# Performance work log

Hardware: AMD Instinct MI355X
Metric: run time of the kernel (lower is better)

## Reference

```python
import jax, jax.numpy as jnp
import numpy as np

BATCH, FEAT, NUM, K = 8, 512, 512, 32

def _l2norm(v, axis):
    # matches F.normalize(p=2): v / max(||v||, eps)
    n = jnp.sqrt(jnp.sum(v * v, axis=axis, keepdims=True))
    return v / jnp.maximum(n, 1e-12)

def setup_inputs() -> dict:
    key = jax.random.key(0)
    k1, k2, k3, k4 = jax.random.split(key, 4)
    x = jax.random.normal(k1, (BATCH, FEAT, NUM), dtype=jnp.float32)
    W = jax.random.normal(k2, (K, FEAT), dtype=jnp.float32) * 0.02
    b = jnp.zeros((K,), dtype=jnp.float32)
    mu = jax.random.uniform(k3, (FEAT, K), dtype=jnp.float32)
    # sigma drawn away from 0 to keep the 1/sigma division well-conditioned
    sigma = jax.random.uniform(k4, (FEAT, K), dtype=jnp.float32, minval=0.5, maxval=1.0)
    return {"x": x, "W": W, "b": b, "mu": mu, "sigma": sigma}

def reference(x, W, b, mu, sigma):
    batch, feat, num = x.shape
    xt = jnp.transpose(x, (0, 2, 1))                      # [b, n, f]
    a = jax.nn.softmax(xt @ W.T + b, axis=2)              # [b, n, k]
    # Fused reduction over n: f = (x - mu)/sigma, fv1 = sum_n a*f, fv2 = sum_n a*(f^2-1)
    asum = jnp.sum(a, axis=1)                             # [b, k]
    ax = jnp.einsum('bnk,bnf->bfk', a, xt)                # sum_n a * x
    ax2 = jnp.einsum('bnk,bnf->bfk', a, xt * xt)          # sum_n a * x^2
    mu_b = mu[None]                                       # [1, f, k]
    sig_b = sigma[None]
    asum_b = asum[:, None, :]                             # [b, 1, k]
    fv1 = (ax - mu_b * asum_b) / sig_b                    # [b, f, k]
    fv2 = (ax2 - 2.0 * mu_b * ax + mu_b * mu_b * asum_b) / (sig_b * sig_b) - asum_b
    fv1 = _l2norm(fv1, 2).reshape(batch, -1)
    fv1 = _l2norm(fv1, 1)
    fv2 = _l2norm(fv2, 2).reshape(batch, -1)
    fv2 = _l2norm(fv2, 1)
    return jnp.concatenate([fv1, fv2], axis=1)            # [b, 2*f*k]
```

## Files before the change

### kernel.cpp

```cpp
#include <hip/hip_runtime.h>


#define B_ 8
#define F_ 512
#define N_ 512
#define K_ 32

__global__ __launch_bounds__(256) void k_a(const float* __restrict__ x,
                                           const float* __restrict__ W,
                                           const float* __restrict__ bias,
                                           float* __restrict__ aP,
                                           float* __restrict__ asumP) {
  __shared__ float xs[128][18];
  __shared__ float ws[128 * 32];
  __shared__ float red2[16][516];
  __shared__ float sm4[4][32];
  const int t = threadIdx.x;
  const int b  = blockIdx.x >> 5;
  const int nt = blockIdx.x & 31;
  const int n0 = nt << 4;
  const int ng = t & 3;
  const int kg = (t >> 2) & 3;
  const int fs = t >> 4;
  const int n4 = ng * 4;
  const int k8 = kg * 8;

  float acc[4][8];
#pragma unroll
  for (int i = 0; i < 4; ++i)
#pragma unroll
    for (int j = 0; j < 8; ++j) acc[i][j] = 0.f;

  float xr[8], wr[16];
#pragma unroll
  for (int it = 0; it < 8; ++it) {
    int flat = t + 256 * it;
    xr[it] = x[(size_t)(b * F_ + (flat >> 4)) * N_ + n0 + (flat & 15)];
  }
#pragma unroll
  for (int it = 0; it < 16; ++it) {
    int flat = t + 256 * it;
    wr[it] = W[(flat >> 7) * F_ + (flat & 127)];
  }
#pragma unroll
  for (int it = 0; it < 8; ++it) {
    int flat = t + 256 * it;
    xs[flat >> 4][flat & 15] = xr[it];
  }
#pragma unroll
  for (int it = 0; it < 16; ++it) {
    int flat = t + 256 * it;
    int f = flat & 127, k = flat >> 7;
    ws[f * 32 + (k ^ (f & 31))] = wr[it];
  }
  __syncthreads();

  for (int ph = 0; ph < 4; ++ph) {
    if (ph < 3) {
      const int fb = (ph + 1) << 7;
#pragma unroll
      for (int it = 0; it < 8; ++it) {
        int flat = t + 256 * it;
        xr[it] = x[(size_t)(b * F_ + fb + (flat >> 4)) * N_ + n0 + (flat & 15)];
      }
#pragma unroll
      for (int it = 0; it < 16; ++it) {
        int flat = t + 256 * it;
        wr[it] = W[(flat >> 7) * F_ + fb + (flat & 127)];
      }
    }
#pragma unroll
    for (int fi = 0; fi < 8; ++fi) {
      const int f = fs * 8 + fi;
      const float2 x01 = *(const float2*)&xs[f][n4];
      const float2 x23 = *(const float2*)&xs[f][n4 + 2];
      const float4 wA = *(const float4*)&ws[f * 32 + ((k8) ^ (f & 28))];
      const float4 wB = *(const float4*)&ws[f * 32 + ((k8 + 4) ^ (f & 28))];
      const float xv[4] = {x01.x, x01.y, x23.x, x23.y};
      const float wa[4] = {((const float*)&wA)[0 ^ (fi & 3)],
                           ((const float*)&wA)[1 ^ (fi & 3)],
                           ((const float*)&wA)[2 ^ (fi & 3)],
                           ((const float*)&wA)[3 ^ (fi & 3)]};
      const float wb[4] = {((const float*)&wB)[0 ^ (fi & 3)],
                           ((const float*)&wB)[1 ^ (fi & 3)],
                           ((const float*)&wB)[2 ^ (fi & 3)],
                           ((const float*)&wB)[3 ^ (fi & 3)]};
#pragma unroll
      for (int i = 0; i < 4; ++i)
#pragma unroll
        for (int j = 0; j < 4; ++j) {
          acc[i][j]     += xv[i] * wa[j];
          acc[i][4 + j] += xv[i] * wb[j];
        }
    }
    __syncthreads();
    if (ph < 3) {
#pragma unroll
      for (int it = 0; it < 8; ++it) {
        int flat = t + 256 * it;
        xs[flat >> 4][flat & 15] = xr[it];
      }
#pragma unroll
      for (int it = 0; it < 16; ++it) {
        int flat = t + 256 * it;
        int f = flat & 127, k = flat >> 7;
        ws[f * 32 + (k ^ (f & 31))] = wr[it];
      }
      __syncthreads();
    }
  }

#pragma unroll
  for (int i = 0; i < 4; ++i) {
    float4 v1, v2;
    v1.x = acc[i][0]; v1.y = acc[i][1]; v1.z = acc[i][2]; v1.w = acc[i][3];
    v2.x = acc[i][4]; v2.y = acc[i][5]; v2.z = acc[i][6]; v2.w = acc[i][7];
    *(float4*)&red2[fs][(n4 + i) * 32 + k8] = v1;
    *(float4*)&red2[fs][(n4 + i) * 32 + k8 + 4] = v2;
  }
  __syncthreads();

  const int o0 = 2 * t;
  const int row = t >> 4;
  const int k0 = o0 & 31;
  float l0 = bias[k0], l1 = bias[k0 + 1];
#pragma unroll
  for (int s2 = 0; s2 < 16; ++s2) {
    float2 r = *(const float2*)&red2[s2][o0];
    l0 += r.x; l1 += r.y;
  }
  float m = fmaxf(l0, l1);
  m = fmaxf(m, __shfl_xor(m, 1));
  m = fmaxf(m, __shfl_xor(m, 2));
  m = fmaxf(m, __shfl_xor(m, 4));
  m = fmaxf(m, __shfl_xor(m, 8));
  const float e0 = __expf(l0 - m), e1 = __expf(l1 - m);
  float ssum = e0 + e1;
  ssum += __shfl_xor(ssum, 1);
  ssum += __shfl_xor(ssum, 2);
  ssum += __shfl_xor(ssum, 4);
  ssum += __shfl_xor(ssum, 8);
  const float inv = 1.f / ssum;
  const float a0 = e0 * inv, a1 = e1 * inv;
  float2 av; av.x = a0; av.y = a1;
  *(float2*)&aP[(size_t)(b * N_ + n0 + row) * K_ + k0] = av;

  float s0 = a0 + __shfl_xor(a0, 16); s0 += __shfl_xor(s0, 32);
  float s1 = a1 + __shfl_xor(a1, 16); s1 += __shfl_xor(s1, 32);
  const int l = t & 63, w = t >> 6;
  if (l < 16) { sm4[w][2 * l] = s0; sm4[w][2 * l + 1] = s1; }
  __syncthreads();
  if (t < 32) {
    float tot = sm4[0][t] + sm4[1][t] + sm4[2][t] + sm4[3][t];
    asumP[(b * 32 + nt) * 32 + t] = tot;
  }
}

__global__ __launch_bounds__(256) void k_ax(const float* __restrict__ x,
                                            const float* __restrict__ aP,
                                            float* __restrict__ axP,
                                            float* __restrict__ ax2P) {
  __shared__ float xsT[64 * 128];
  __shared__ float as_[64][36];
  const int t  = threadIdx.x;
  const int s  = blockIdx.x & 7;
  const int ft = (blockIdx.x >> 3) & 3;
  const int b  = blockIdx.x >> 5;
  const int f0 = ft << 7;
  const int n0 = s << 6;
  const int fg = t >> 3, kg = t & 7;
  const int f4 = fg * 4, k4 = kg * 4;

#pragma unroll
  for (int it = 0; it < 32; ++it) {
    int flat = t + 256 * it;
    int f = flat >> 6, nn = flat & 63;
    xsT[nn * 128 + (f ^ (nn & 31))] =
        x[(size_t)(b * F_ + f0 + f) * N_ + n0 + nn];
  }
#pragma unroll
  for (int it = 0; it < 8; ++it) {
    int flat = t + 256 * it;
    int r = flat >> 5, kk = flat & 31;
    as_[r][kk] = aP[(size_t)(b * N_ + n0 + r) * K_ + kk];
  }
  __syncthreads();

  float ax[4][4] = {{0.f}}, bx[4][4] = {{0.f}};
#pragma unroll 2
  for (int nb = 0; nb < 64; nb += 4) {
#pragma unroll
    for (int u = 0; u < 4; ++u) {
      const int n = nb + u;
      const float4 xv = *(const float4*)&xsT[n * 128 + (f4 ^ (n & 28))];
      const float4 av = *(const float4*)&as_[n][k4];
      const float* xp = (const float*)&xv;
      const float* ap = (const float*)&av;
#pragma unroll
      for (int i = 0; i < 4; ++i) {
        const float xi = xp[i ^ u];
        const float xq = xi * xi;
#pragma unroll
        for (int j = 0; j < 4; ++j) {
          ax[i][j] += xi * ap[j];
          bx[i][j] += xq * ap[j];
        }
      }
    }
  }

  const size_t pbase = ((size_t)(s * B_ + b) * F_ + f0 + f4) * K_ + k4;
#pragma unroll
  for (int i = 0; i < 4; ++i) {
    float4 v1, v2;
    v1.x = ax[i][0]; v1.y = ax[i][1]; v1.z = ax[i][2]; v1.w = ax[i][3];
    v2.x = bx[i][0]; v2.y = bx[i][1]; v2.z = bx[i][2]; v2.w = bx[i][3];
    *(float4*)&axP [pbase + (size_t)i * K_] = v1;
    *(float4*)&ax2P[pbase + (size_t)i * K_] = v2;
  }
}

__global__ __launch_bounds__(256) void k_fv(const float* __restrict__ axP,
                                            const float* __restrict__ ax2P,
                                            const float* __restrict__ asumP,
                                            const float* __restrict__ mu,
                                            const float* __restrict__ sg,
                                            float* __restrict__ out) {
  __shared__ float sm[32];
  const int t = threadIdx.x;
  const int g = blockIdx.x * 256 + t;
  const int k = g & 31;
  const int f = (g >> 5) & (F_ - 1);
  const int b = g >> 14;

  if (t < 32) {
    float s = 0.f;
#pragma unroll
    for (int nt = 0; nt < 32; ++nt) s += asumP[(b * 32 + nt) * 32 + t];
    sm[t] = s;
  }
  __syncthreads();

  float ax = 0.f, ax2 = 0.f;
#pragma unroll
  for (int s = 0; s < 8; ++s) {
    ax  += axP [(size_t)((s * B_ + b) * F_ + f) * K_ + k];
    ax2 += ax2P[(size_t)((s * B_ + b) * F_ + f) * K_ + k];
  }
  const float m  = mu[f * K_ + k];
  const float sd = sg[f * K_ + k];
  const float as = sm[k];

  const float fv1 = (ax - m * as) / sd;
  const float fv2 = (ax2 - 2.f * m * ax + m * m * as) / (sd * sd) - as;

  float s1 = fv1 * fv1, s2 = fv2 * fv2;
#pragma unroll
  for (int off = 16; off >= 1; off >>= 1) {
    s1 += __shfl_xor(s1, off, 32);
    s2 += __shfl_xor(s2, off, 32);
  }
  const float inv512 = 0.04419417382415922f;
  const float o1 = fv1 / fmaxf(sqrtf(s1), 1e-12f) * inv512;
  const float o2 = fv2 / fmaxf(sqrtf(s2), 1e-12f) * inv512;

  out[(size_t)b * (2 * F_ * K_) + f * K_ + k] = o1;
  out[(size_t)b * (2 * F_ * K_) + F_ * K_ + f * K_ + k] = o2;
}

extern "C" void kernel_launch(void* const* d_in, const int* in_sizes, int n_in,
                              void* d_out, int out_size, void* d_ws, size_t ws_size,
                              hipStream_t stream) {
  const float* x  = (const float*)d_in[0];
  const float* W  = (const float*)d_in[1];
  const float* bv = (const float*)d_in[2];
  const float* mu = (const float*)d_in[3];
  const float* sg = (const float*)d_in[4];
  float* out = (float*)d_out;

  float* ws    = (float*)d_ws;
  float* aP    = ws;
  float* axP   = ws + 131072;
  float* ax2P  = ws + 131072 + 1048576;
  float* asumP = ws + 131072 + 2 * 1048576;

  hipLaunchKernelGGL(k_a,  dim3(256), dim3(256), 0, stream, x, W, bv, aP, asumP);
  hipLaunchKernelGGL(k_ax, dim3(256), dim3(256), 0, stream, x, aP, axP, ax2P);
  hipLaunchKernelGGL(k_fv, dim3(512), dim3(256), 0, stream,
                     axP, ax2P, asumP, mu, sg, out);
}
```

Baseline: 85.78 us.

## Fuse weighted-moment reduction with Fisher-vector normalization into one kernel

Merges the k_ax and k_fv kernels into a single k_axfv kernel. Each block now owns 8 features of one batch and loops over all 512 points in chunks of 128, register-prefetching the next chunk of x and the soft-assignment matrix while the current one is computed. Per-thread partials are reduced in shared memory, then normalized and written directly. This removes the 8-way split-N partial buffers, the global round-trip between the two kernels and one launch. In exchange, each block rereads the full per-batch assignment matrix (64 blocks per batch) and gets less parallelism per block along N.

```diff
diff --git a/kernel.cpp b/kernel.cpp
--- a/kernel.cpp
+++ b/kernel.cpp
@@ -156,49 +156,75 @@
   }
 }
 
-__global__ __launch_bounds__(256) void k_ax(const float* __restrict__ x,
-                                            const float* __restrict__ aP,
-                                            float* __restrict__ axP,
-                                            float* __restrict__ ax2P) {
-  __shared__ float xsT[64 * 128];
-  __shared__ float as_[64][36];
+__global__ __launch_bounds__(256) void k_axfv(const float* __restrict__ x,
+                                              const float* __restrict__ aP,
+                                              const float* __restrict__ asumP,
+                                              const float* __restrict__ mu,
+                                              const float* __restrict__ sg,
+                                              float* __restrict__ out) {
+  __shared__ float pool[8448];
+  __shared__ float sm[32];
+  float* xs  = pool;
+  float* as_ = pool + 1056;
   const int t  = threadIdx.x;
-  const int s  = blockIdx.x & 7;
-  const int ft = (blockIdx.x >> 3) & 3;
-  const int b  = blockIdx.x >> 5;
-  const int f0 = ft << 7;
-  const int n0 = s << 6;
-  const int fg = t >> 3, kg = t & 7;
-  const int f4 = fg * 4, k4 = kg * 4;
-
-#pragma unroll
-  for (int it = 0; it < 32; ++it) {
-    int flat = t + 256 * it;
-    int f = flat >> 6, nn = flat & 63;
-    xsT[nn * 128 + (f ^ (nn & 31))] =
-        x[(size_t)(b * F_ + f0 + f) * N_ + n0 + nn];
-  }
-#pragma unroll
-  for (int it = 0; it < 8; ++it) {
-    int flat = t + 256 * it;
-    int r = flat >> 5, kk = flat & 31;
-    as_[r][kk] = aP[(size_t)(b * N_ + n0 + r) * K_ + kk];
-  }
-  __syncthreads();
+  const int b  = blockIdx.x >> 6;
+  const int ft = blockIdx.x & 63;
+  const int f0 = ft << 3;
+  const int kg = t & 7;
+  const int fg = (t >> 3) & 1;
+  const int ns = t >> 4;
+  const int k4 = kg * 4;
+  const int f4 = fg * 4;
+
+  if (t < 32) {
+    float s = 0.f;
+#pragma unroll
+    for (int nt = 0; nt < 32; ++nt) s += asumP[(b * 32 + nt) * 32 + t];
+    sm[t] = s;
+  }
 
   float ax[4][4] = {{0.f}}, bx[4][4] = {{0.f}};
-#pragma unroll 2
-  for (int nb = 0; nb < 64; nb += 4) {
-#pragma unroll
-    for (int u = 0; u < 4; ++u) {
-      const int n = nb + u;
-      const float4 xv = *(const float4*)&xsT[n * 128 + (f4 ^ (n & 28))];
-      const float4 av = *(const float4*)&as_[n][k4];
-      const float* xp = (const float*)&xv;
+  float xr[4], ar[16];
+#pragma unroll
+  for (int it = 0; it < 4; ++it) {
+    int flat = t + 256 * it;
+    xr[it] = x[(size_t)(b * F_ + f0 + (flat >> 7)) * N_ + (flat & 127)];
+  }
+#pragma unroll
+  for (int it = 0; it < 16; ++it)
+    ar[it] = aP[(size_t)b * N_ * K_ + t + 256 * it];
+#pragma unroll
+  for (int it = 0; it < 4; ++it) {
+    int flat = t + 256 * it;
+    xs[(flat >> 7) * 132 + (flat & 127)] = xr[it];
+  }
+#pragma unroll
+  for (int it = 0; it < 16; ++it) as_[t + 256 * it] = ar[it];
+  __syncthreads();
+
+  for (int c = 0; c < 4; ++c) {
+    if (c < 3) {
+      const int nc = (c + 1) << 7;
+#pragma unroll
+      for (int it = 0; it < 4; ++it) {
+        int flat = t + 256 * it;
+        xr[it] = x[(size_t)(b * F_ + f0 + (flat >> 7)) * N_ + nc + (flat & 127)];
+      }
+#pragma unroll
+      for (int it = 0; it < 16; ++it)
+        ar[it] = aP[(size_t)b * N_ * K_ + nc * K_ + t + 256 * it];
+    }
+#pragma unroll
+    for (int u = 0; u < 8; ++u) {
+      const int n = ns * 8 + u;
+      const float4 av = *(const float4*)&as_[n * 32 + k4];
       const float* ap = (const float*)&av;
+      float xv[4];
+#pragma unroll
+      for (int i = 0; i < 4; ++i) xv[i] = xs[(f4 + i) * 132 + n];
 #pragma unroll
       for (int i = 0; i < 4; ++i) {
-        const float xi = xp[i ^ u];
+        const float xi = xv[i];
         const float xq = xi * xi;
 #pragma unroll
         for (int j = 0; j < 4; ++j) {
@@ -207,52 +233,43 @@
         }
       }
     }
-  }
-
-  const size_t pbase = ((size_t)(s * B_ + b) * F_ + f0 + f4) * K_ + k4;
+    __syncthreads();
+    if (c < 3) {
+#pragma unroll
+      for (int it = 0; it < 4; ++it) {
+        int flat = t + 256 * it;
+        xs[(flat >> 7) * 132 + (flat & 127)] = xr[it];
+      }
+#pragma unroll
+      for (int it = 0; it < 16; ++it) as_[t + 256 * it] = ar[it];
+      __syncthreads();
+    }
+  }
+
 #pragma unroll
   for (int i = 0; i < 4; ++i) {
     float4 v1, v2;
     v1.x = ax[i][0]; v1.y = ax[i][1]; v1.z = ax[i][2]; v1.w = ax[i][3];
     v2.x = bx[i][0]; v2.y = bx[i][1]; v2.z = bx[i][2]; v2.w = bx[i][3];
-    *(float4*)&axP [pbase + (size_t)i * K_] = v1;
-    *(float4*)&ax2P[pbase + (size_t)i * K_] = v2;
-  }
-}
-
-__global__ __launch_bounds__(256) void k_fv(const float* __restrict__ axP,
-                                            const float* __restrict__ ax2P,
-                                            const float* __restrict__ asumP,
-                                            const float* __restrict__ mu,
-                                            const float* __restrict__ sg,
-                                            float* __restrict__ out) {
-  __shared__ float sm[32];
-  const int t = threadIdx.x;
-  const int g = blockIdx.x * 256 + t;
-  const int k = g & 31;
-  const int f = (g >> 5) & (F_ - 1);
-  const int b = g >> 14;
-
-  if (t < 32) {
-    float s = 0.f;
-#pragma unroll
-    for (int nt = 0; nt < 32; ++nt) s += asumP[(b * 32 + nt) * 32 + t];
-    sm[t] = s;
-  }
-  __syncthreads();
-
-  float ax = 0.f, ax2 = 0.f;
-#pragma unroll
-  for (int s = 0; s < 8; ++s) {
-    ax  += axP [(size_t)((s * B_ + b) * F_ + f) * K_ + k];
-    ax2 += ax2P[(size_t)((s * B_ + b) * F_ + f) * K_ + k];
-  }
-  const float m  = mu[f * K_ + k];
-  const float sd = sg[f * K_ + k];
-  const float as = sm[k];
-
-  const float fv1 = (ax - m * as) / sd;
-  const float fv2 = (ax2 - 2.f * m * ax + m * m * as) / (sd * sd) - as;
+    *(float4*)&pool[ns * 264 + (f4 + i) * 32 + k4] = v1;
+    *(float4*)&pool[4224 + ns * 264 + (f4 + i) * 32 + k4] = v2;
+  }
+  __syncthreads();
+
+  const int fr = t >> 5;
+  const int kr = t & 31;
+  float axv = 0.f, a2v = 0.f;
+#pragma unroll
+  for (int p = 0; p < 16; ++p) {
+    axv += pool[p * 264 + fr * 32 + kr];
+    a2v += pool[4224 + p * 264 + fr * 32 + kr];
+  }
+  const float m  = mu[(f0 + fr) * K_ + kr];
+  const float sd = sg[(f0 + fr) * K_ + kr];
+  const float as = sm[kr];
+
+  const float fv1 = (axv - m * as) / sd;
+  const float fv2 = (a2v - 2.f * m * axv + m * m * as) / (sd * sd) - as;
 
   float s1 = fv1 * fv1, s2 = fv2 * fv2;
 #pragma unroll
@@ -264,8 +281,8 @@
   const float o1 = fv1 / fmaxf(sqrtf(s1), 1e-12f) * inv512;
   const float o2 = fv2 / fmaxf(sqrtf(s2), 1e-12f) * inv512;
 
-  out[(size_t)b * (2 * F_ * K_) + f * K_ + k] = o1;
-  out[(size_t)b * (2 * F_ * K_) + F_ * K_ + f * K_ + k] = o2;
+  out[(size_t)b * (2 * F_ * K_) + (f0 + fr) * K_ + kr] = o1;
+  out[(size_t)b * (2 * F_ * K_) + F_ * K_ + (f0 + fr) * K_ + kr] = o2;
 }
 
 extern "C" void kernel_launch(void* const* d_in, const int* in_sizes, int n_in,
@@ -280,12 +297,9 @@
 
   float* ws    = (float*)d_ws;
   float* aP    = ws;
-  float* axP   = ws + 131072;
-  float* ax2P  = ws + 131072 + 1048576;
-  float* asumP = ws + 131072 + 2 * 1048576;
-
-  hipLaunchKernelGGL(k_a,  dim3(256), dim3(256), 0, stream, x, W, bv, aP, asumP);
-  hipLaunchKernelGGL(k_ax, dim3(256), dim3(256), 0, stream, x, aP, axP, ax2P);
-  hipLaunchKernelGGL(k_fv, dim3(512), dim3(256), 0, stream,
-                     axP, ax2P, asumP, mu, sg, out);
+  float* asumP = ws + 131072;
+
+  hipLaunchKernelGGL(k_a,    dim3(256), dim3(256), 0, stream, x, W, bv, aP, asumP);
+  hipLaunchKernelGGL(k_axfv, dim3(512), dim3(256), 0, stream,
+                     x, aP, asumP, mu, sg, out);
 }
```

New measurement: 80.91 us. -5.7%, faster.
